# Performance work log

Measured on AMD Instinct MI355X. Metric: run time of the kernel, lower is better.

Reference implementation:

```python
import jax, jax.numpy as jnp
import numpy as np

B_, H_, N_, L_ = 4, 512, 64, 2048  # batch, d_model, d_state/2 (conj pairs), seq len


def setup_inputs() -> dict:
    key = jax.random.key(0)
    ks = jax.random.split(key, 8)
    x = jax.random.normal(ks[0], (B_, H_, L_), jnp.float32)
    ln_w = jnp.ones((H_,), jnp.float32)
    ln_b = jnp.zeros((H_,), jnp.float32)
    # S4D-style init: dt log-uniform in [1e-3, 1e-1], A = -1/2 + i*pi*n (S4D-Lin)
    log_dt = jax.random.uniform(ks[1], (H_,), jnp.float32) * (np.log(0.1) - np.log(0.001)) + np.log(0.001)
    log_A_real = jnp.broadcast_to(jnp.log(jnp.float32(0.5)), (H_, N_))
    A_imag = jnp.broadcast_to(np.pi * jnp.arange(N_, dtype=np.float32), (H_, N_))
    B_re = jnp.ones((H_, N_), jnp.float32)
    B_im = jnp.zeros((H_, N_), jnp.float32)
    # 2 kernel channels for bidirectional
    C_re = jax.random.normal(ks[2], (2, H_, N_), jnp.float32) * (0.5 ** 0.5)
    C_im = jax.random.normal(ks[3], (2, H_, N_), jnp.float32) * (0.5 ** 0.5)
    D = jax.random.normal(ks[4], (H_,), jnp.float32)
    W_out = jax.random.normal(ks[5], (H_, H_), jnp.float32) / np.sqrt(H_)
    b_out = jnp.zeros((H_,), jnp.float32)
    return dict(x=x, ln_w=ln_w, ln_b=ln_b, log_dt=log_dt, log_A_real=log_A_real,
                A_imag=A_imag, B_re=B_re, B_im=B_im, C_re=C_re, C_im=C_im,
                D=D, W_out=W_out, b_out=b_out)


def _s4_layer(x, ln_w, ln_b, log_dt, log_A_real, A_imag, B_re, B_im, C_re, C_im, D, W_out, b_out):
    Bb, H, L = x.shape
    # ---- pre-norm LayerNorm over channel dim (module transposes to (B,L,H)) ----
    zt = x.transpose(0, 2, 1)                          # (B, L, H)
    mu = zt.mean(-1, keepdims=True)
    var = jnp.mean((zt - mu) ** 2, -1, keepdims=True)
    zt = (zt - mu) * jax.lax.rsqrt(var + 1e-5) * ln_w + ln_b
    z = zt.transpose(0, 2, 1)                          # (B, H, L)
    # ---- S4 diagonal SSM kernel, ZOH discretization, 2 channels (bidirectional) ----
    dt = jnp.exp(log_dt)[:, None]                      # (H, 1)
    A = -jnp.exp(log_A_real) + 1j * A_imag             # (H, N)
    dtA = A * dt                                       # (H, N)
    dB = (B_re + 1j * B_im) * (jnp.exp(dtA) - 1.0) / A # (H, N) discretized B
    CB = (C_re + 1j * C_im) * dB                       # (2, H, N)
    V = jnp.exp(dtA[:, :, None] * jnp.arange(L))       # (H, N, L) Vandermonde exp(l*dt*A)
    k = 2.0 * jnp.real(jnp.einsum('chn,hnl->chl', CB, V))  # (2, H, L)
    # ---- bidirectional: causal + flipped anticausal kernel, length 2L ----
    zpad = jnp.zeros_like(k[0])
    kb = jnp.concatenate([k[0], zpad], -1) + jnp.concatenate([zpad, k[1][:, ::-1]], -1)  # (H, 2L)
    # ---- FFT convolution ----
    k_f = jnp.fft.rfft(kb, n=2 * L)                    # (H, L+1)
    u_f = jnp.fft.rfft(z, n=2 * L)                     # (B, H, L+1)
    y = jnp.fft.irfft(u_f * k_f, n=2 * L)[..., :L]     # (B, H, L)
    y = y + z * D[:, None]                             # skip connection D*u
    y = jax.nn.gelu(y)                                 # default S4 activation
    y = jnp.einsum('oh,bhl->bol', W_out, y) + b_out[:, None]  # output linear (Conv1d k=1)
    return y + x                                       # residual of S4Layer


def reference(x, ln_w, ln_b, log_dt, log_A_real, A_imag, B_re, B_im, C_re, C_im, D, W_out, b_out):
    return _s4_layer(x, ln_w, ln_b, log_dt, log_A_real, A_imag, B_re, B_im, C_re, C_im, D, W_out, b_out)
```

## Files before the change

### kernel.cpp

```cpp
#include <hip/hip_runtime.h>
#include <math.h>

#define Bq 4
#define Hq 512
#define Nq 64
#define Lq 2048
#define PARAM (Hq*Nq)
#define T 64
#define NC (Lq/T)
#define NCOL 256

__global__ void prep_kernel(const float* __restrict__ log_dt,
                            const float* __restrict__ log_A_real,
                            const float* __restrict__ A_imag,
                            const float* __restrict__ B_re, const float* __restrict__ B_im,
                            const float* __restrict__ C_re, const float* __restrict__ C_im,
                            float* __restrict__ wr_, float* __restrict__ wi_,
                            float* __restrict__ a0, float* __restrict__ b0,
                            float* __restrict__ a1, float* __restrict__ b1) {
    int idx = blockIdx.x * blockDim.x + threadIdx.x;
    if (idx >= PARAM) return;
    int h = idx >> 6;
    float dt = expf(log_dt[h]);
    float Ar = -expf(log_A_real[idx]);
    float Ai = A_imag[idx];
    float er = expf(Ar * dt);
    float wr = er * cosf(Ai * dt);
    float wi = er * sinf(Ai * dt);
    wr_[idx] = wr; wi_[idx] = wi;
    float mr = wr - 1.0f, mi = wi;
    float den = Ar * Ar + Ai * Ai;
    float qr = (mr * Ar + mi * Ai) / den;
    float qi = (mi * Ar - mr * Ai) / den;
    float Br = B_re[idx], Bi = B_im[idx];
    float dBr = Br * qr - Bi * qi;
    float dBi = Br * qi + Bi * qr;
    float cr = C_re[idx], ci = C_im[idx];
    a0[idx] =  2.0f * (cr * dBr - ci * dBi);
    b0[idx] = -2.0f * (cr * dBi + ci * dBr);
    cr = C_re[PARAM + idx]; ci = C_im[PARAM + idx];
    a1[idx] =  2.0f * (cr * dBr - ci * dBi);
    b1[idx] = -2.0f * (cr * dBi + ci * dBr);
}

__global__ __launch_bounds__(256)
void ln_kernel(const float* __restrict__ x, const float* __restrict__ lnw,
               const float* __restrict__ lnb, float* __restrict__ z) {
    int blk = blockIdx.x;
    int b  = blk / (Lq / 16);
    int l0 = (blk % (Lq / 16)) * 16;
    int tx = threadIdx.x & 15;
    int ty = threadIdx.x >> 4;
    const float* xb = x + (size_t)b * Hq * Lq;
    float s = 0.f, s2 = 0.f;
    for (int h = ty; h < Hq; h += 16) {
        float v = xb[h * Lq + l0 + tx];
        s += v; s2 += v * v;
    }
    __shared__ float rs_[16][17], r2_[16][17], mu_s[16], sg_s[16];
    rs_[ty][tx] = s; r2_[ty][tx] = s2;
    __syncthreads();
    if (ty == 0) {
        float a = 0.f, c = 0.f;
        #pragma unroll
        for (int i = 0; i < 16; ++i) { a += rs_[i][tx]; c += r2_[i][tx]; }
        float mu = a * (1.0f / Hq);
        float var = c * (1.0f / Hq) - mu * mu;
        mu_s[tx] = mu;
        sg_s[tx] = rsqrtf(var + 1e-5f);
    }
    __syncthreads();
    float mu = mu_s[tx], rs = sg_s[tx];
    float* zb = z + (size_t)b * Hq * Lq;
    for (int h = ty; h < Hq; h += 16) {
        float v = xb[h * Lq + l0 + tx];
        zb[h * Lq + l0 + tx] = (v - mu) * rs * lnw[h] + lnb[h];
    }
}


__global__ __launch_bounds__(256)
void delta_kernel(const float* __restrict__ z,
                  const float* __restrict__ wr_, const float* __restrict__ wi_,
                  float* __restrict__ buf) {
    __shared__ float powc[64][64], pows[64][64];
    __shared__ float Bs[64][68];
    int h = blockIdx.x, ct = blockIdx.y;
    int t = threadIdx.x;
    if (t < 64) {
        float wr = wr_[h*64+t], wi = wi_[h*64+t];
        float c = 1.f, s = 0.f;
        for (int d = 0; d < 64; ++d) {
            powc[d][t] = c; pows[d][t] = s;
            float nc = c*wr - s*wi, ns = c*wi + s*wr;
            c = nc; s = ns;
        }
    }
    {
        int dir = ct >> 1;
        int r = t >> 7, tt = t & 127;
        int b = (ct & 1)*2 + r;
        int l = tt * 16;
        int c0 = l >> 6, j0 = l & 63;
        const float* zb = z + ((size_t)b*Hq + h)*Lq;
        int cc = r*32 + c0;
        if (dir == 0) {
            #pragma unroll
            for (int q = 0; q < 4; ++q)
                *(float4*)&Bs[cc][j0+4*q] = *(const float4*)(zb + c0*64 + j0 + 4*q);
        } else {
            #pragma unroll
            for (int q = 0; q < 4; ++q) {
                float4 v = *(const float4*)(zb + 2044 - c0*64 - (j0+4*q));
                float4 w; w.x = v.w; w.y = v.z; w.z = v.y; w.w = v.x;
                *(float4*)&Bs[cc][j0+4*q] = w;
            }
        }
    }
    __syncthreads();
    int cg = t & 15, rg = t >> 4;
    int n0 = 4*rg;
    float aR[4][4] = {}, aI[4][4] = {};
    #pragma unroll 4
    for (int j = 0; j < 64; ++j) {
        int d = 63 - j;
        float4 pc = *(const float4*)&powc[d][n0];
        float4 ps = *(const float4*)&pows[d][n0];
        float bz[4];
        #pragma unroll
        for (int q = 0; q < 4; ++q) bz[q] = Bs[cg + 16*q][j];
        #pragma unroll
        for (int nn = 0; nn < 4; ++nn) {
            float pcv = (&pc.x)[nn], psv = (&ps.x)[nn];
            #pragma unroll
            for (int q = 0; q < 4; ++q) {
                aR[nn][q] = fmaf(pcv, bz[q], aR[nn][q]);
                aI[nn][q] = fmaf(psv, bz[q], aI[nn][q]);
            }
        }
    }
    #pragma unroll
    for (int q = 0; q < 4; ++q) {
        int col = ct*64 + cg + 16*q;
        float* dst = buf + ((size_t)h*NCOL + col)*128 + 2*n0;
        float4 v1, v2;
        v1.x = aR[0][q]; v1.y = aI[0][q]; v1.z = aR[1][q]; v1.w = aI[1][q];
        v2.x = aR[2][q]; v2.y = aI[2][q]; v2.z = aR[3][q]; v2.w = aI[3][q];
        *(float4*)dst = v1; *(float4*)(dst+4) = v2;
    }
}

__global__ __launch_bounds__(256)
void cscan_kernel(const float* __restrict__ wr_, const float* __restrict__ wi_,
                  float* __restrict__ buf) {
    int e = blockIdx.x*4 + (threadIdx.x >> 6);
    int n = threadIdx.x & 63;
    int h = e >> 3, dir = (e >> 2) & 1, b = e & 3;
    float wr = wr_[h*64+n], wi = wi_[h*64+n];
    double cr = wr, ci = wi;
    #pragma unroll
    for (int q = 0; q < 6; ++q) {
        double nr = cr*cr - ci*ci, ni = 2.0*cr*ci;
        cr = nr; ci = ni;
    }
    float tc = (float)cr, ts = (float)ci;
    float sr = 0.f, si = 0.f;
    float2* p = (float2*)(buf + ((size_t)h*NCOL + dir*128 + b*32)*128) + n;
    float2 d = p[0];
    for (int c = 0; c < NC; ++c) {
        float2 dn;
        if (c + 1 < NC) dn = p[(c+1)*64];
        float2 s; s.x = sr; s.y = si;
        p[c*64] = s;
        float nr = fmaf(tc, sr, fmaf(-ts, si, d.x));
        float ni = fmaf(ts, sr, fmaf(tc, si, d.y));
        sr = nr; si = ni; d = dn;
    }
}

__global__ __launch_bounds__(256)
void y_kernel(const float* __restrict__ z,
              const float* __restrict__ wr_, const float* __restrict__ wi_,
              const float* __restrict__ a0, const float* __restrict__ b0,
              const float* __restrict__ a1, const float* __restrict__ b1,
              const float* __restrict__ buf,
              float* __restrict__ y0, float* __restrict__ y1) {
    __shared__ float powc[64][64], pows[64][64];
    __shared__ float As[32][64];
    __shared__ float Bs[64][36];
    __shared__ float ks[64], as_[64], bs_[64];
    int h = blockIdx.x, dir = blockIdx.y, ct = blockIdx.z;
    int t = threadIdx.x;
    const float* aa = dir ? a1 : a0;
    const float* bb = dir ? b1 : b0;
    if (t < 64) {
        float wr = wr_[h*64+t], wi = wi_[h*64+t];
        as_[t] = aa[h*64+t]; bs_[t] = bb[h*64+t];
        float c, s;
        if (dir == 0) { c = wr; s = wi; } else { c = 1.f; s = 0.f; }
        for (int d = 0; d < 64; ++d) {
            powc[d][t] = c; pows[d][t] = s;
            float nc = c*wr - s*wi, ns = c*wi + s*wr;
            c = nc; s = ns;
        }
    }
    __syncthreads();
    if (t < 64) {
        int d = t;
        float acc = 0.f;
        if (dir == 0 && d == 0) {
            for (int st = 0; st < 64; ++st) acc += as_[(st + d) & 63];
        } else {
            int row = (dir == 0) ? d - 1 : d;
            for (int st = 0; st < 64; ++st) {
                int n = (st + d) & 63;
                acc = fmaf(as_[n], powc[row][n], acc);
                acc = fmaf(bs_[n], pows[row][n], acc);
            }
        }
        ks[d] = acc;
    }
    __syncthreads();
    int tx = t & 15, ty = t >> 4;
    float acc[4][4] = {};
    for (int p = 0; p < 6; ++p) {
        {
            int kk = t & 31, ig = t >> 5;
            if (p < 2) {
                int j = 32*p + kk;
                int off = (dir == 0) ? 0 : 1;
                #pragma unroll
                for (int ii = 0; ii < 8; ++ii) {
                    int i = ig*8 + ii;
                    int idx = i - j - off;
                    As[kk][i] = (idx >= 0) ? ks[idx] : 0.f;
                }
            } else {
                int m = 32*(p-2) + kk;
                int n = m >> 1;
                float av = as_[n], bv = bs_[n];
                if ((m & 1) == 0) {
                    #pragma unroll
                    for (int ii = 0; ii < 8; ++ii) {
                        int i = ig*8 + ii;
                        As[kk][i] = fmaf(av, powc[i][n], bv*pows[i][n]);
                    }
                } else {
                    #pragma unroll
                    for (int ii = 0; ii < 8; ++ii) {
                        int i = ig*8 + ii;
                        As[kk][i] = fmaf(bv, powc[i][n], -av*pows[i][n]);
                    }
                }
            }
        }
        {
            int cc = t >> 2, q = t & 3;
            int colg = ct*64 + cc;
            int b = colg >> 5, c = colg & 31;
            int kk0 = q*8;
            if (p < 2) {
                const float* zb = z + ((size_t)b*Hq + h)*Lq;
                int j0 = 32*p + kk0;
                if (dir == 0) {
                    *(float4*)&Bs[cc][kk0]   = *(const float4*)(zb + c*64 + j0);
                    *(float4*)&Bs[cc][kk0+4] = *(const float4*)(zb + c*64 + j0 + 4);
                } else {
                    float4 v = *(const float4*)(zb + 2044 - c*64 - j0);
                    float4 w; w.x=v.w; w.y=v.z; w.z=v.y; w.w=v.x;
                    *(float4*)&Bs[cc][kk0] = w;
                    v = *(const float4*)(zb + 2044 - c*64 - (j0+4));
                    w.x=v.w; w.y=v.z; w.z=v.y; w.w=v.x;
                    *(float4*)&Bs[cc][kk0+4] = w;
                }
            } else {
                int m0 = 32*(p-2) + kk0;
                int col = dir*128 + colg;
                const float* src = buf + ((size_t)h*NCOL + col)*128 + m0;
                *(float4*)&Bs[cc][kk0]   = *(const float4*)src;
                *(float4*)&Bs[cc][kk0+4] = *(const float4*)(src+4);
            }
        }
        __syncthreads();
        #pragma unroll 8
        for (int kk = 0; kk < 32; ++kk) {
            float4 av = *(const float4*)&As[kk][4*tx];
            float bv0 = Bs[4*ty+0][kk], bv1 = Bs[4*ty+1][kk];
            float bv2 = Bs[4*ty+2][kk], bv3 = Bs[4*ty+3][kk];
            #pragma unroll
            for (int ii = 0; ii < 4; ++ii) {
                float a = (&av.x)[ii];
                acc[ii][0] = fmaf(a, bv0, acc[ii][0]);
                acc[ii][1] = fmaf(a, bv1, acc[ii][1]);
                acc[ii][2] = fmaf(a, bv2, acc[ii][2]);
                acc[ii][3] = fmaf(a, bv3, acc[ii][3]);
            }
        }
        __syncthreads();
    }
    #pragma unroll
    for (int q = 0; q < 4; ++q) {
        int colg = ct*64 + 4*ty + q;
        int b = colg >> 5, c = colg & 31;
        float4 v;
        if (dir == 0) {
            v.x = acc[0][q]; v.y = acc[1][q]; v.z = acc[2][q]; v.w = acc[3][q];
            *(float4*)(y0 + ((size_t)b*Hq + h)*Lq + c*64 + 4*tx) = v;
        } else {
            v.x = acc[3][q]; v.y = acc[2][q]; v.z = acc[1][q]; v.w = acc[0][q];
            *(float4*)(y1 + ((size_t)b*Hq + h)*Lq + 2044 - c*64 - 4*tx) = v;
        }
    }
}

__global__ __launch_bounds__(256)
void act_kernel(float4* __restrict__ y0, const float4* __restrict__ y1,
                const float4* __restrict__ z, const float* __restrict__ D) {
    int i4 = blockIdx.x * 256 + threadIdx.x;
    int h = (i4 >> 9) & (Hq - 1);
    float d = D[h];
    float4 v0 = y0[i4], v1 = y1[i4], vz = z[i4];
    float vv[4] = { v0.x + v1.x + d * vz.x, v0.y + v1.y + d * vz.y,
                    v0.z + v1.z + d * vz.z, v0.w + v1.w + d * vz.w };
    #pragma unroll
    for (int i = 0; i < 4; ++i) {
        float v = vv[i];
        float tt = tanhf(0.7978845608028654f * (v + 0.044715f * v * v * v));
        vv[i] = 0.5f * v * (1.0f + tt);
    }
    float4 r; r.x = vv[0]; r.y = vv[1]; r.z = vv[2]; r.w = vv[3];
    y0[i4] = r;
}

__global__ __launch_bounds__(256)
void gemm_kernel(const float* __restrict__ u, const float* __restrict__ W,
                 const float* __restrict__ bias, const float* __restrict__ x,
                 float* __restrict__ out) {
    int l0 = blockIdx.x * 64;
    int o0 = blockIdx.y * 128;
    int b  = blockIdx.z;
    int tid = threadIdx.x;
    __shared__ float Ws[16][129];
    __shared__ float Us[16][65];
    const float* ub = u + (size_t)b * Hq * Lq;
    float acc[8][4] = {};
    int wo = tid >> 4, wl = tid & 15;
    for (int k0 = 0; k0 < Hq; k0 += 16) {
        {
            int j  = tid & 15;
            int ib = tid >> 4;
            #pragma unroll
            for (int r = 0; r < 8; ++r) {
                int i = ib + 16 * r;
                Ws[j][i] = W[(size_t)(o0 + i) * Hq + k0 + j];
            }
            int li = tid & 63;
            int jb = tid >> 6;
            #pragma unroll
            for (int r = 0; r < 4; ++r) {
                int j2 = jb + 4 * r;
                Us[j2][li] = ub[(size_t)(k0 + j2) * Lq + l0 + li];
            }
        }
        __syncthreads();
        #pragma unroll
        for (int j = 0; j < 16; ++j) {
            float av[8], bv[4];
            #pragma unroll
            for (int i = 0; i < 8; ++i) av[i] = Ws[j][8 * wo + i];
            #pragma unroll
            for (int i = 0; i < 4; ++i) bv[i] = Us[j][4 * wl + i];
            #pragma unroll
            for (int io = 0; io < 8; ++io)
                #pragma unroll
                for (int il = 0; il < 4; ++il)
                    acc[io][il] = fmaf(av[io], bv[il], acc[io][il]);
        }
        __syncthreads();
    }
    #pragma unroll
    for (int io = 0; io < 8; ++io) {
        int o = o0 + 8 * wo + io;
        float bo = bias[o];
        size_t base = ((size_t)b * Hq + o) * Lq + l0 + 4 * wl;
        const float4 xr = *(const float4*)(x + base);
        float4 r;
        r.x = acc[io][0] + bo + xr.x;
        r.y = acc[io][1] + bo + xr.y;
        r.z = acc[io][2] + bo + xr.z;
        r.w = acc[io][3] + bo + xr.w;
        *(float4*)(out + base) = r;
    }
}

extern "C" void kernel_launch(void* const* d_in, const int* in_sizes, int n_in,
                              void* d_out, int out_size, void* d_ws, size_t ws_size,
                              hipStream_t stream) {
    (void)in_sizes; (void)n_in; (void)out_size; (void)ws_size;
    const float* x          = (const float*)d_in[0];
    const float* ln_w       = (const float*)d_in[1];
    const float* ln_b       = (const float*)d_in[2];
    const float* log_dt     = (const float*)d_in[3];
    const float* log_A_real = (const float*)d_in[4];
    const float* A_imag     = (const float*)d_in[5];
    const float* B_re       = (const float*)d_in[6];
    const float* B_im       = (const float*)d_in[7];
    const float* C_re       = (const float*)d_in[8];
    const float* C_im       = (const float*)d_in[9];
    const float* Dv         = (const float*)d_in[10];
    const float* W          = (const float*)d_in[11];
    const float* b_out      = (const float*)d_in[12];
    float* out = (float*)d_out;
    float* ws  = (float*)d_ws;

    const size_t BHL = (size_t)Bq * Hq * Lq;
    float* wr  = ws;
    float* wi  = ws + PARAM;
    float* a0  = ws + 2 * (size_t)PARAM;
    float* b0  = ws + 3 * (size_t)PARAM;
    float* a1  = ws + 4 * (size_t)PARAM;
    float* b1  = ws + 5 * (size_t)PARAM;
    float* z   = ws + 6 * (size_t)PARAM;
    float* y0  = z  + BHL;
    float* y1  = y0 + BHL;
    float* buf = y1 + BHL;

    prep_kernel<<<PARAM / 256, 256, 0, stream>>>(log_dt, log_A_real, A_imag,
                                                 B_re, B_im, C_re, C_im,
                                                 wr, wi, a0, b0, a1, b1);
    ln_kernel<<<Bq * (Lq / 16), 256, 0, stream>>>(x, ln_w, ln_b, z);
    delta_kernel<<<dim3(Hq, 4), 256, 0, stream>>>(z, wr, wi, buf);
    cscan_kernel<<<Bq * Hq * 2 / 4, 256, 0, stream>>>(wr, wi, buf);
    y_kernel<<<dim3(Hq, 2, 2), 256, 0, stream>>>(z, wr, wi, a0, b0, a1, b1,
                                                 buf, y0, y1);
    act_kernel<<<(Bq * Hq * Lq / 4) / 256, 256, 0, stream>>>((float4*)y0, (const float4*)y1,
                                                             (const float4*)z, Dv);
    gemm_kernel<<<dim3(Lq / 64, Hq / 128, Bq), 256, 0, stream>>>(y0, W, b_out, x, out);
}
```

Before: 324.3 us.

## Precompute power tables and kernel taps once in global memory, transpose LDS tiles

Powers w^d (d=0..64) are computed once in prep_kernel and stored in a global table, which delta, cscan and y kernels now read. Previously each block recomputed them serially into shared memory, and cscan squared in double precision. A new ktap_kernel computes the 64 kernel taps per head and direction once instead of per block. Shared tiles are transposed so the inner loops use float4 LDS reads, shared memory shrinks, and launch bounds raise occupancy. The cost is an extra launch and a few MB of global table traffic, plus a small precision change from iterated float powers replacing double squaring.

```diff
diff --git a/kernel.cpp b/kernel.cpp
--- a/kernel.cpp
+++ b/kernel.cpp
@@ -15,19 +15,18 @@
                             const float* __restrict__ A_imag,
                             const float* __restrict__ B_re, const float* __restrict__ B_im,
                             const float* __restrict__ C_re, const float* __restrict__ C_im,
-                            float* __restrict__ wr_, float* __restrict__ wi_,
                             float* __restrict__ a0, float* __restrict__ b0,
-                            float* __restrict__ a1, float* __restrict__ b1) {
+                            float* __restrict__ a1, float* __restrict__ b1,
+                            float* __restrict__ pw) {
     int idx = blockIdx.x * blockDim.x + threadIdx.x;
     if (idx >= PARAM) return;
-    int h = idx >> 6;
+    int h = idx >> 6, n = idx & 63;
     float dt = expf(log_dt[h]);
     float Ar = -expf(log_A_real[idx]);
     float Ai = A_imag[idx];
     float er = expf(Ar * dt);
     float wr = er * cosf(Ai * dt);
     float wi = er * sinf(Ai * dt);
-    wr_[idx] = wr; wi_[idx] = wi;
     float mr = wr - 1.0f, mi = wi;
     float den = Ar * Ar + Ai * Ai;
     float qr = (mr * Ar + mi * Ai) / den;
@@ -41,6 +40,34 @@
     cr = C_re[PARAM + idx]; ci = C_im[PARAM + idx];
     a1[idx] =  2.0f * (cr * dBr - ci * dBi);
     b1[idx] = -2.0f * (cr * dBi + ci * dBr);
+    float c = 1.f, s = 0.f;
+    float* base = pw + (size_t)h * 65 * 128 + 2 * n;
+    for (int d = 0; d <= 64; ++d) {
+        *(float2*)(base + (size_t)d * 128) = float2{c, s};
+        float nc = c * wr - s * wi;
+        float ns = c * wi + s * wr;
+        c = nc; s = ns;
+    }
+}
+
+__global__ __launch_bounds__(128)
+void ktap_kernel(const float* __restrict__ pw,
+                 const float* __restrict__ a0, const float* __restrict__ b0,
+                 const float* __restrict__ a1, const float* __restrict__ b1,
+                 float* __restrict__ kt) {
+    int h = blockIdx.x;
+    int t = threadIdx.x;
+    int dir = t >> 6, d = t & 63;
+    const float* aa = dir ? a1 : a0;
+    const float* bb = dir ? b1 : b0;
+    const float* row = pw + (size_t)(h * 65 + d) * 128;
+    float acc = 0.f;
+    for (int n = 0; n < 64; ++n) {
+        float2 v = *(const float2*)(row + 2 * n);
+        acc = fmaf(aa[h * 64 + n], v.x, acc);
+        acc = fmaf(bb[h * 64 + n], v.y, acc);
+    }
+    kt[((size_t)h * 2 + dir) * 64 + d] = acc;
 }
 
 __global__ __launch_bounds__(256)
@@ -79,236 +106,191 @@
 }
 
 
-__global__ __launch_bounds__(256)
-void delta_kernel(const float* __restrict__ z,
-                  const float* __restrict__ wr_, const float* __restrict__ wi_,
+__global__ __launch_bounds__(256, 6)
+void delta_kernel(const float* __restrict__ z, const float* __restrict__ pw,
                   float* __restrict__ buf) {
-    __shared__ float powc[64][64], pows[64][64];
     __shared__ float Bs[64][68];
     int h = blockIdx.x, ct = blockIdx.y;
     int t = threadIdx.x;
-    if (t < 64) {
-        float wr = wr_[h*64+t], wi = wi_[h*64+t];
-        float c = 1.f, s = 0.f;
-        for (int d = 0; d < 64; ++d) {
-            powc[d][t] = c; pows[d][t] = s;
-            float nc = c*wr - s*wi, ns = c*wi + s*wr;
-            c = nc; s = ns;
-        }
-    }
-    {
-        int dir = ct >> 1;
-        int r = t >> 7, tt = t & 127;
-        int b = (ct & 1)*2 + r;
-        int l = tt * 16;
-        int c0 = l >> 6, j0 = l & 63;
-        const float* zb = z + ((size_t)b*Hq + h)*Lq;
-        int cc = r*32 + c0;
-        if (dir == 0) {
-            #pragma unroll
-            for (int q = 0; q < 4; ++q)
-                *(float4*)&Bs[cc][j0+4*q] = *(const float4*)(zb + c0*64 + j0 + 4*q);
-        } else {
+    int dir = ct >> 1;
+    int cc = t & 31, rb = (t >> 5) & 1, jg = t >> 6;
+    int b = (ct & 1) * 2 + rb;
+    const float* zb = z + ((size_t)b * Hq + h) * Lq;
+    if (dir == 0) {
+        #pragma unroll
+        for (int f = 0; f < 4; ++f) {
+            float4 v = *(const float4*)(zb + cc * 64 + 16 * jg + 4 * f);
+            Bs[16*jg+4*f+0][rb*32+cc] = v.x;
+            Bs[16*jg+4*f+1][rb*32+cc] = v.y;
+            Bs[16*jg+4*f+2][rb*32+cc] = v.z;
+            Bs[16*jg+4*f+3][rb*32+cc] = v.w;
+        }
+    } else {
+        #pragma unroll
+        for (int f = 0; f < 4; ++f) {
+            float4 v = *(const float4*)(zb + 2044 - cc * 64 - 16 * jg - 4 * f);
+            Bs[16*jg+4*f+3][rb*32+cc] = v.x;
+            Bs[16*jg+4*f+2][rb*32+cc] = v.y;
+            Bs[16*jg+4*f+1][rb*32+cc] = v.z;
+            Bs[16*jg+4*f+0][rb*32+cc] = v.w;
+        }
+    }
+    __syncthreads();
+    int tx = t & 15, ty = t >> 4;
+    float aR[4][4] = {}, aI[4][4] = {};
+    const float* pwh = pw + (size_t)h * 65 * 128;
+    #pragma unroll 4
+    for (int kk = 0; kk < 64; ++kk) {
+        int d = 63 - kk;
+        const float4* pr = (const float4*)(pwh + (size_t)d * 128 + 8 * tx);
+        float4 p0 = pr[0], p1 = pr[1];
+        float4 bv = *(const float4*)&Bs[kk][4 * ty];
+        float pc[4] = {p0.x, p0.z, p1.x, p1.z};
+        float ps[4] = {p0.y, p0.w, p1.y, p1.w};
+        #pragma unroll
+        for (int rr = 0; rr < 4; ++rr) {
             #pragma unroll
             for (int q = 0; q < 4; ++q) {
-                float4 v = *(const float4*)(zb + 2044 - c0*64 - (j0+4*q));
-                float4 w; w.x = v.w; w.y = v.z; w.z = v.y; w.w = v.x;
-                *(float4*)&Bs[cc][j0+4*q] = w;
-            }
-        }
-    }
-    __syncthreads();
-    int cg = t & 15, rg = t >> 4;
-    int n0 = 4*rg;
-    float aR[4][4] = {}, aI[4][4] = {};
-    #pragma unroll 4
-    for (int j = 0; j < 64; ++j) {
-        int d = 63 - j;
-        float4 pc = *(const float4*)&powc[d][n0];
-        float4 ps = *(const float4*)&pows[d][n0];
-        float bz[4];
-        #pragma unroll
-        for (int q = 0; q < 4; ++q) bz[q] = Bs[cg + 16*q][j];
-        #pragma unroll
-        for (int nn = 0; nn < 4; ++nn) {
-            float pcv = (&pc.x)[nn], psv = (&ps.x)[nn];
-            #pragma unroll
-            for (int q = 0; q < 4; ++q) {
-                aR[nn][q] = fmaf(pcv, bz[q], aR[nn][q]);
-                aI[nn][q] = fmaf(psv, bz[q], aI[nn][q]);
+                aR[rr][q] = fmaf(pc[rr], (&bv.x)[q], aR[rr][q]);
+                aI[rr][q] = fmaf(ps[rr], (&bv.x)[q], aI[rr][q]);
             }
         }
     }
     #pragma unroll
     for (int q = 0; q < 4; ++q) {
-        int col = ct*64 + cg + 16*q;
-        float* dst = buf + ((size_t)h*NCOL + col)*128 + 2*n0;
+        int colg = ct * 64 + 4 * ty + q;
+        float* dst = buf + ((size_t)h * NCOL + colg) * 128 + 8 * tx;
         float4 v1, v2;
         v1.x = aR[0][q]; v1.y = aI[0][q]; v1.z = aR[1][q]; v1.w = aI[1][q];
         v2.x = aR[2][q]; v2.y = aI[2][q]; v2.z = aR[3][q]; v2.w = aI[3][q];
-        *(float4*)dst = v1; *(float4*)(dst+4) = v2;
+        *(float4*)dst = v1; *(float4*)(dst + 4) = v2;
     }
 }
 
 __global__ __launch_bounds__(256)
-void cscan_kernel(const float* __restrict__ wr_, const float* __restrict__ wi_,
-                  float* __restrict__ buf) {
-    int e = blockIdx.x*4 + (threadIdx.x >> 6);
+void cscan_kernel(const float* __restrict__ pw, float* __restrict__ buf) {
+    int e = blockIdx.x * 4 + (threadIdx.x >> 6);
     int n = threadIdx.x & 63;
     int h = e >> 3, dir = (e >> 2) & 1, b = e & 3;
-    float wr = wr_[h*64+n], wi = wi_[h*64+n];
-    double cr = wr, ci = wi;
-    #pragma unroll
-    for (int q = 0; q < 6; ++q) {
-        double nr = cr*cr - ci*ci, ni = 2.0*cr*ci;
-        cr = nr; ci = ni;
-    }
-    float tc = (float)cr, ts = (float)ci;
+    float2 t64 = *(const float2*)(pw + (size_t)(h * 65 + 64) * 128 + 2 * n);
+    float tc = t64.x, ts = t64.y;
     float sr = 0.f, si = 0.f;
-    float2* p = (float2*)(buf + ((size_t)h*NCOL + dir*128 + b*32)*128) + n;
+    float2* p = (float2*)(buf + ((size_t)h * NCOL + dir * 128 + b * 32) * 128) + n;
     float2 d = p[0];
     for (int c = 0; c < NC; ++c) {
         float2 dn;
-        if (c + 1 < NC) dn = p[(c+1)*64];
+        if (c + 1 < NC) dn = p[(c + 1) * 64];
         float2 s; s.x = sr; s.y = si;
-        p[c*64] = s;
+        p[c * 64] = s;
         float nr = fmaf(tc, sr, fmaf(-ts, si, d.x));
         float ni = fmaf(ts, sr, fmaf(tc, si, d.y));
         sr = nr; si = ni; d = dn;
     }
 }
 
-__global__ __launch_bounds__(256)
-void y_kernel(const float* __restrict__ z,
-              const float* __restrict__ wr_, const float* __restrict__ wi_,
+__global__ __launch_bounds__(256, 8)
+void y_kernel(const float* __restrict__ z, const float* __restrict__ pw,
               const float* __restrict__ a0, const float* __restrict__ b0,
               const float* __restrict__ a1, const float* __restrict__ b1,
-              const float* __restrict__ buf,
+              const float* __restrict__ kt, const float* __restrict__ buf,
               float* __restrict__ y0, float* __restrict__ y1) {
-    __shared__ float powc[64][64], pows[64][64];
-    __shared__ float As[32][64];
-    __shared__ float Bs[64][36];
+    __shared__ float As[32][68];
+    __shared__ float Bs[32][68];
     __shared__ float ks[64], as_[64], bs_[64];
     int h = blockIdx.x, dir = blockIdx.y, ct = blockIdx.z;
     int t = threadIdx.x;
-    const float* aa = dir ? a1 : a0;
-    const float* bb = dir ? b1 : b0;
     if (t < 64) {
-        float wr = wr_[h*64+t], wi = wi_[h*64+t];
-        as_[t] = aa[h*64+t]; bs_[t] = bb[h*64+t];
-        float c, s;
-        if (dir == 0) { c = wr; s = wi; } else { c = 1.f; s = 0.f; }
-        for (int d = 0; d < 64; ++d) {
-            powc[d][t] = c; pows[d][t] = s;
-            float nc = c*wr - s*wi, ns = c*wi + s*wr;
-            c = nc; s = ns;
-        }
-    }
+        ks[t]  = kt[((size_t)h * 2 + dir) * 64 + t];
+        as_[t] = (dir ? a1 : a0)[h * 64 + t];
+        bs_[t] = (dir ? b1 : b0)[h * 64 + t];
+    }
+    int tx = t & 15, ty = t >> 4;
+    int si = t & 63, sg = t >> 6;
+    int cc = t & 31, rb = (t >> 5) & 1, kg = t >> 6;
+    int b = ct * 2 + rb;
+    const float* zb = z + ((size_t)b * Hq + h) * Lq;
+    int off = (dir == 0) ? 1 : 0;
+    const float* prow = pw + (size_t)(h * 65 + si + off) * 128;
+    float acc[4][4] = {};
     __syncthreads();
-    if (t < 64) {
-        int d = t;
-        float acc = 0.f;
-        if (dir == 0 && d == 0) {
-            for (int st = 0; st < 64; ++st) acc += as_[(st + d) & 63];
+    for (int p = 0; p < 6; ++p) {
+        if (p < 2) {
+            #pragma unroll
+            for (int q = 0; q < 8; ++q) {
+                int kk = 8 * sg + q;
+                int j = 32 * p + kk;
+                int idx = (dir == 0) ? (si - j) : (si - j - 1);
+                As[kk][si] = (idx >= 0) ? ks[idx] : 0.f;
+            }
         } else {
-            int row = (dir == 0) ? d - 1 : d;
-            for (int st = 0; st < 64; ++st) {
-                int n = (st + d) & 63;
-                acc = fmaf(as_[n], powc[row][n], acc);
-                acc = fmaf(bs_[n], pows[row][n], acc);
-            }
-        }
-        ks[d] = acc;
-    }
-    __syncthreads();
-    int tx = t & 15, ty = t >> 4;
-    float acc[4][4] = {};
-    for (int p = 0; p < 6; ++p) {
-        {
-            int kk = t & 31, ig = t >> 5;
-            if (p < 2) {
-                int j = 32*p + kk;
-                int off = (dir == 0) ? 0 : 1;
+            #pragma unroll
+            for (int q = 0; q < 8; ++q) {
+                int kk = 8 * sg + q;
+                int m = 32 * (p - 2) + kk;
+                int n = m >> 1;
+                float2 v = *(const float2*)(prow + 2 * n);
+                float av = as_[n], bv = bs_[n];
+                As[kk][si] = ((m & 1) == 0) ? fmaf(av, v.x, bv * v.y)
+                                            : fmaf(bv, v.x, -av * v.y);
+            }
+        }
+        if (p < 2) {
+            if (dir == 0) {
                 #pragma unroll
-                for (int ii = 0; ii < 8; ++ii) {
-                    int i = ig*8 + ii;
-                    int idx = i - j - off;
-                    As[kk][i] = (idx >= 0) ? ks[idx] : 0.f;
+                for (int f = 0; f < 2; ++f) {
+                    float4 v = *(const float4*)(zb + cc * 64 + 32 * p + 8 * kg + 4 * f);
+                    Bs[8*kg+4*f+0][rb*32+cc] = v.x;
+                    Bs[8*kg+4*f+1][rb*32+cc] = v.y;
+                    Bs[8*kg+4*f+2][rb*32+cc] = v.z;
+                    Bs[8*kg+4*f+3][rb*32+cc] = v.w;
                 }
             } else {
-                int m = 32*(p-2) + kk;
-                int n = m >> 1;
-                float av = as_[n], bv = bs_[n];
-                if ((m & 1) == 0) {
-                    #pragma unroll
-                    for (int ii = 0; ii < 8; ++ii) {
-                        int i = ig*8 + ii;
-                        As[kk][i] = fmaf(av, powc[i][n], bv*pows[i][n]);
-                    }
-                } else {
-                    #pragma unroll
-                    for (int ii = 0; ii < 8; ++ii) {
-                        int i = ig*8 + ii;
-                        As[kk][i] = fmaf(bv, powc[i][n], -av*pows[i][n]);
-                    }
+                #pragma unroll
+                for (int f = 0; f < 2; ++f) {
+                    float4 v = *(const float4*)(zb + 2044 - cc * 64 - 32 * p - 8 * kg - 4 * f);
+                    Bs[8*kg+4*f+3][rb*32+cc] = v.x;
+                    Bs[8*kg+4*f+2][rb*32+cc] = v.y;
+                    Bs[8*kg+4*f+1][rb*32+cc] = v.z;
+                    Bs[8*kg+4*f+0][rb*32+cc] = v.w;
                 }
             }
-        }
-        {
-            int cc = t >> 2, q = t & 3;
-            int colg = ct*64 + cc;
-            int b = colg >> 5, c = colg & 31;
-            int kk0 = q*8;
-            if (p < 2) {
-                const float* zb = z + ((size_t)b*Hq + h)*Lq;
-                int j0 = 32*p + kk0;
-                if (dir == 0) {
-                    *(float4*)&Bs[cc][kk0]   = *(const float4*)(zb + c*64 + j0);
-                    *(float4*)&Bs[cc][kk0+4] = *(const float4*)(zb + c*64 + j0 + 4);
-                } else {
-                    float4 v = *(const float4*)(zb + 2044 - c*64 - j0);
-                    float4 w; w.x=v.w; w.y=v.z; w.z=v.y; w.w=v.x;
-                    *(float4*)&Bs[cc][kk0] = w;
-                    v = *(const float4*)(zb + 2044 - c*64 - (j0+4));
-                    w.x=v.w; w.y=v.z; w.z=v.y; w.w=v.x;
-                    *(float4*)&Bs[cc][kk0+4] = w;
-                }
-            } else {
-                int m0 = 32*(p-2) + kk0;
-                int col = dir*128 + colg;
-                const float* src = buf + ((size_t)h*NCOL + col)*128 + m0;
-                *(float4*)&Bs[cc][kk0]   = *(const float4*)src;
-                *(float4*)&Bs[cc][kk0+4] = *(const float4*)(src+4);
-            }
+        } else {
+            int colg = dir * 128 + ct * 64 + rb * 32 + cc;
+            const float* src = buf + ((size_t)h * NCOL + colg) * 128 + 32 * (p - 2) + 8 * kg;
+            float4 v0 = *(const float4*)src;
+            float4 v1 = *(const float4*)(src + 4);
+            #pragma unroll
+            for (int e2 = 0; e2 < 4; ++e2) Bs[8*kg+e2][rb*32+cc]   = (&v0.x)[e2];
+            #pragma unroll
+            for (int e2 = 0; e2 < 4; ++e2) Bs[8*kg+4+e2][rb*32+cc] = (&v1.x)[e2];
         }
         __syncthreads();
         #pragma unroll 8
         for (int kk = 0; kk < 32; ++kk) {
-            float4 av = *(const float4*)&As[kk][4*tx];
-            float bv0 = Bs[4*ty+0][kk], bv1 = Bs[4*ty+1][kk];
-            float bv2 = Bs[4*ty+2][kk], bv3 = Bs[4*ty+3][kk];
+            float4 av = *(const float4*)&As[kk][4 * tx];
+            float4 bv = *(const float4*)&Bs[kk][4 * ty];
             #pragma unroll
             for (int ii = 0; ii < 4; ++ii) {
                 float a = (&av.x)[ii];
-                acc[ii][0] = fmaf(a, bv0, acc[ii][0]);
-                acc[ii][1] = fmaf(a, bv1, acc[ii][1]);
-                acc[ii][2] = fmaf(a, bv2, acc[ii][2]);
-                acc[ii][3] = fmaf(a, bv3, acc[ii][3]);
+                acc[ii][0] = fmaf(a, bv.x, acc[ii][0]);
+                acc[ii][1] = fmaf(a, bv.y, acc[ii][1]);
+                acc[ii][2] = fmaf(a, bv.z, acc[ii][2]);
+                acc[ii][3] = fmaf(a, bv.w, acc[ii][3]);
             }
         }
         __syncthreads();
     }
     #pragma unroll
     for (int q = 0; q < 4; ++q) {
-        int colg = ct*64 + 4*ty + q;
-        int b = colg >> 5, c = colg & 31;
+        int coll = 4 * ty + q;
+        int bo = ct * 2 + (coll >> 5), c = coll & 31;
         float4 v;
         if (dir == 0) {
             v.x = acc[0][q]; v.y = acc[1][q]; v.z = acc[2][q]; v.w = acc[3][q];
-            *(float4*)(y0 + ((size_t)b*Hq + h)*Lq + c*64 + 4*tx) = v;
+            *(float4*)(y0 + ((size_t)bo * Hq + h) * Lq + c * 64 + 4 * tx) = v;
         } else {
             v.x = acc[3][q]; v.y = acc[2][q]; v.z = acc[1][q]; v.w = acc[0][q];
-            *(float4*)(y1 + ((size_t)b*Hq + h)*Lq + 2044 - c*64 - 4*tx) = v;
+            *(float4*)(y1 + ((size_t)bo * Hq + h) * Lq + 2044 - c * 64 - 4 * tx) = v;
         }
     }
 }
@@ -414,25 +396,26 @@
     float* ws  = (float*)d_ws;
 
     const size_t BHL = (size_t)Bq * Hq * Lq;
-    float* wr  = ws;
-    float* wi  = ws + PARAM;
-    float* a0  = ws + 2 * (size_t)PARAM;
-    float* b0  = ws + 3 * (size_t)PARAM;
-    float* a1  = ws + 4 * (size_t)PARAM;
-    float* b1  = ws + 5 * (size_t)PARAM;
-    float* z   = ws + 6 * (size_t)PARAM;
+    float* a0  = ws;
+    float* b0  = ws + (size_t)PARAM;
+    float* a1  = ws + 2 * (size_t)PARAM;
+    float* b1  = ws + 3 * (size_t)PARAM;
+    float* kt  = ws + 4 * (size_t)PARAM;
+    float* pw  = ws + 6 * (size_t)PARAM;
+    float* z   = ws + 136 * (size_t)PARAM;
     float* y0  = z  + BHL;
     float* y1  = y0 + BHL;
     float* buf = y1 + BHL;
 
     prep_kernel<<<PARAM / 256, 256, 0, stream>>>(log_dt, log_A_real, A_imag,
                                                  B_re, B_im, C_re, C_im,
-                                                 wr, wi, a0, b0, a1, b1);
+                                                 a0, b0, a1, b1, pw);
     ln_kernel<<<Bq * (Lq / 16), 256, 0, stream>>>(x, ln_w, ln_b, z);
-    delta_kernel<<<dim3(Hq, 4), 256, 0, stream>>>(z, wr, wi, buf);
-    cscan_kernel<<<Bq * Hq * 2 / 4, 256, 0, stream>>>(wr, wi, buf);
-    y_kernel<<<dim3(Hq, 2, 2), 256, 0, stream>>>(z, wr, wi, a0, b0, a1, b1,
-                                                 buf, y0, y1);
+    ktap_kernel<<<Hq, 128, 0, stream>>>(pw, a0, b0, a1, b1, kt);
+    delta_kernel<<<dim3(Hq, 4), 256, 0, stream>>>(z, pw, buf);
+    cscan_kernel<<<Bq * Hq * 2 / 4, 256, 0, stream>>>(pw, buf);
+    y_kernel<<<dim3(Hq, 2, 2), 256, 0, stream>>>(z, pw, a0, b0, a1, b1,
+                                                 kt, buf, y0, y1);
     act_kernel<<<(Bq * Hq * Lq / 4) / 256, 256, 0, stream>>>((float4*)y0, (const float4*)y1,
                                                              (const float4*)z, Dv);
     gemm_kernel<<<dim3(Lq / 64, Hq / 128, Bq), 256, 0, stream>>>(y0, W, b_out, x, out);
```

Result: slower. 331.8 us (+2.3%).
